# Optimization experiments

Hardware: AMD Instinct MI355X
Metric: run time of the kernel (lower is better)

Reference implementation:

```python
import jax, jax.numpy as jnp
import numpy as np

KSZ = 7
PAD = 3


def setup_inputs() -> dict:
    key = jax.random.key(0)
    ks = jax.random.split(key, 5)
    b, t, c, h, w = 8, 16, 256, 28, 28
    x = jax.random.normal(ks[0], (b, t, c, h, w), dtype=jnp.float32)
    W1 = jax.random.normal(ks[1], (2 * t, t), dtype=jnp.float32) * 0.1
    W2 = jax.random.normal(ks[2], (KSZ, 2 * t), dtype=jnp.float32) * 0.1
    Wl1 = jax.random.normal(ks[3], (c // 4, c, KSZ), dtype=jnp.float32) * 0.05
    Wl2 = jax.random.normal(ks[4], (c, c // 4, 1), dtype=jnp.float32) * 0.1
    return {"x": x, "W1": W1, "W2": W2, "Wl1": Wl1, "Wl2": Wl2}


def _tam_forward(x, W1, W2, Wl1, Wl2):
    b, t, c, h, w = x.shape
    xp = jnp.transpose(x, (0, 2, 1, 3, 4))  # [b,c,t,h,w]
    pooled = jnp.mean(xp, axis=(3, 4))       # [b,c,t] (adaptive_avg_pool2d to 1x1)

    # G branch: per-(b,c) dynamic 7-tap softmax kernel
    g = jnp.tanh(jnp.einsum('bct,ut->bcu', pooled, W1))
    kernel = jax.nn.softmax(jnp.einsum('bcu,ku->bck', g, W2), axis=-1)  # [b,c,7]

    # L branch: conv1d(c -> c/4, k=7, pad=3) -> tanh -> conv1d(c/4 -> c, k=1) -> sigmoid
    y = jax.lax.conv_general_dilated(
        pooled, Wl1, window_strides=(1,), padding=[(PAD, PAD)],
        dimension_numbers=('NCH', 'OIH', 'NCH'))
    y = jnp.tanh(y)  # [b, c/4, t]
    local = jax.nn.sigmoid(jnp.einsum('oi,bit->bot', Wl2[:, :, 0], y))  # [b,c,t]

    gated = xp * local[:, :, :, None, None]  # [b,c,t,h,w]

    # Depthwise temporal conv (groups = b*c), stride 1, pad 3 on t
    padded = jnp.pad(gated, ((0, 0), (0, 0), (PAD, PAD), (0, 0), (0, 0)))
    out = jnp.zeros_like(gated)
    for k in range(KSZ):
        out = out + kernel[:, :, k, None, None, None] * padded[:, :, k:k + t]
    out = jnp.transpose(out, (0, 2, 1, 3, 4))  # [b,t,c,h,w]
    return out.reshape(b * t, c, h, w)


def reference(x, W1, W2, Wl1, Wl2):
    return _tam_forward(x, W1, W2, Wl1, Wl2)
```

## Files before the change

### kernel.cpp

```cpp
#include <hip/hip_runtime.h>

constexpr int B_  = 8;
constexpr int T_  = 16;
constexpr int C_  = 256;
constexpr int HW_ = 784;
constexpr int CO_ = 64;
constexpr int K_  = 7;
constexpr int U2_ = 32;

typedef float floatx4 __attribute__((ext_vector_type(4)));

__device__ __forceinline__ float rfl(float v) {
    return __int_as_float(__builtin_amdgcn_readfirstlane(__float_as_int(v)));
}

__global__ __launch_bounds__(256) void pool_kernel(const float* __restrict__ x,
                                                   float* __restrict__ pooled) {
    int bid  = blockIdx.x;
    int cg   = bid & 63;
    int bt   = bid >> 6;
    int t    = bt & 15;
    int b    = bt >> 4;
    int wave = threadIdx.x >> 6;
    int lane = threadIdx.x & 63;
    int c    = cg * 4 + wave;

    const floatx4* p4 = (const floatx4*)(x + ((size_t)bt * C_ + c) * HW_);
    float s = 0.f;
    for (int j = lane; j < 196; j += 64) {
        floatx4 v = p4[j];
        s += (v.x + v.y) + (v.z + v.w);
    }
#pragma unroll
    for (int m = 32; m >= 1; m >>= 1) s += __shfl_xor(s, m, 64);
    if (lane == 0) pooled[((size_t)b * C_ + c) * T_ + t] = s * (1.0f / 784.0f);
}

__global__ __launch_bounds__(256) void ty_kernel(const float* __restrict__ pooled,
                                                 const float* __restrict__ Wl1,
                                                 float* __restrict__ ty) {
    int b = blockIdx.x / CO_;
    int o = blockIdx.x % CO_;
    __shared__ float pld[T_ * 257];

    int tid = threadIdx.x;
    for (int idx = tid; idx < C_ * T_; idx += 256) {
        int i  = idx >> 4;
        int tt = idx & 15;
        pld[tt * 257 + i] = pooled[((size_t)b * C_ + i) * T_ + tt];
    }
    __syncthreads();

    int t = tid >> 4;
    int q = tid & 15;
    const float* wrow = Wl1 + (size_t)o * (C_ * K_);
    float acc = 0.f;
    for (int j = 0; j < 16; ++j) {
        int i = j * 16 + q;
        const float* wp = wrow + i * K_;
#pragma unroll
        for (int k = 0; k < K_; ++k) {
            int tt = t + k - 3;
            if (tt >= 0 && tt < T_) acc += wp[k] * pld[tt * 257 + i];
        }
    }
    acc += __shfl_xor(acc, 1, 64);
    acc += __shfl_xor(acc, 2, 64);
    acc += __shfl_xor(acc, 4, 64);
    acc += __shfl_xor(acc, 8, 64);
    if (q == 0) ty[((size_t)b * CO_ + o) * T_ + t] = tanhf(acc);
}

__global__ __launch_bounds__(256) void stream_coef_kernel(const float* __restrict__ x,
                                                          const float* __restrict__ pooled,
                                                          const float* __restrict__ ty,
                                                          const float* __restrict__ W1,
                                                          const float* __restrict__ W2,
                                                          const float* __restrict__ Wl2,
                                                          float* __restrict__ out) {
    int bc = blockIdx.x;
    int b  = bc >> 8;
    int c  = bc & 255;
    int tid = threadIdx.x;
    bool active = tid < 196;

    const size_t chan = ((size_t)(b * T_) * C_ + c) * HW_ + (size_t)tid * 4;
    const float* xb = x + chan;
    float*       ob = out + chan;
    const size_t ts = (size_t)C_ * HW_;

    floatx4 w[11];
    if (active) {
#pragma unroll
        for (int tp = 0; tp < 11; ++tp)
            w[tp] = *(const floatx4*)(xb + (size_t)tp * ts);
    }

    __shared__ float loc_s[T_];
    __shared__ float g_s[U2_];
    __shared__ float s_s[8];
    __shared__ float kw_s[8];

    {
        int t = tid >> 4, q = tid & 15;
        float acc = 0.f;
#pragma unroll
        for (int jj = 0; jj < 4; ++jj) {
            int o = q + jj * 16;
            acc += Wl2[(size_t)c * CO_ + o] * ty[((size_t)b * CO_ + o) * T_ + t];
        }
        acc += __shfl_xor(acc, 1, 64);
        acc += __shfl_xor(acc, 2, 64);
        acc += __shfl_xor(acc, 4, 64);
        acc += __shfl_xor(acc, 8, 64);
        if (q == 0) loc_s[t] = 1.0f / (1.0f + __expf(-acc));
    }
    if (tid < U2_) {
        float acc = 0.f;
#pragma unroll
        for (int t2 = 0; t2 < T_; ++t2)
            acc += pooled[(size_t)bc * T_ + t2] * W1[tid * T_ + t2];
        g_s[tid] = tanhf(acc);
    }
    __syncthreads();
    if (tid < K_) {
        float acc = 0.f;
#pragma unroll
        for (int u = 0; u < U2_; ++u) acc += g_s[u] * W2[tid * U2_ + u];
        s_s[tid] = acc;
    }
    __syncthreads();
    if (tid == 0) {
        float m = s_s[0];
#pragma unroll
        for (int k = 1; k < K_; ++k) m = fmaxf(m, s_s[k]);
        float e[K_], sum = 0.f;
#pragma unroll
        for (int k = 0; k < K_; ++k) { e[k] = __expf(s_s[k] - m); sum += e[k]; }
        float inv = 1.0f / sum;
#pragma unroll
        for (int k = 0; k < K_; ++k) kw_s[k] = e[k] * inv;
    }
    __syncthreads();

    float kw[K_], lc[T_];
#pragma unroll
    for (int k = 0; k < K_; ++k) kw[k] = rfl(kw_s[k]);
#pragma unroll
    for (int t = 0; t < T_; ++t) lc[t] = rfl(loc_s[t]);

    if (!active) return;

#pragma unroll
    for (int tp = 0; tp < 11; ++tp) w[tp] *= lc[tp];

#pragma unroll
    for (int t = 0; t < 8; ++t) {
        floatx4 acc = {0.f, 0.f, 0.f, 0.f};
#pragma unroll
        for (int d = -3; d <= 3; ++d) {
            int tp = t + d;
            if (tp >= 0 && tp <= 10) acc += kw[d + 3] * w[tp];
        }
        __builtin_nontemporal_store(acc, (floatx4*)(ob + (size_t)t * ts));
    }

#pragma unroll
    for (int j = 0; j < 6; ++j) w[j] = w[5 + j];
#pragma unroll
    for (int tp = 11; tp < 16; ++tp)
        w[tp - 5] = *(const floatx4*)(xb + (size_t)tp * ts) * lc[tp];

#pragma unroll
    for (int t = 8; t < 16; ++t) {
        floatx4 acc = {0.f, 0.f, 0.f, 0.f};
#pragma unroll
        for (int d = -3; d <= 3; ++d) {
            int tp = t + d;
            if (tp <= 15) acc += kw[d + 3] * w[tp - 5];
        }
        __builtin_nontemporal_store(acc, (floatx4*)(ob + (size_t)t * ts));
    }
}

extern "C" void kernel_launch(void* const* d_in, const int* in_sizes, int n_in,
                              void* d_out, int out_size, void* d_ws, size_t ws_size,
                              hipStream_t stream) {
    const float* x   = (const float*)d_in[0];
    const float* W1  = (const float*)d_in[1];
    const float* W2  = (const float*)d_in[2];
    const float* Wl1 = (const float*)d_in[3];
    const float* Wl2 = (const float*)d_in[4];
    float* out = (float*)d_out;

    float* pooled = (float*)d_ws;
    float* ty     = pooled + B_ * C_ * T_;

    pool_kernel<<<B_ * T_ * (C_ / 4), 256, 0, stream>>>(x, pooled);
    ty_kernel<<<B_ * CO_, 256, 0, stream>>>(pooled, Wl1, ty);
    stream_coef_kernel<<<B_ * C_, 256, 0, stream>>>(x, pooled, ty, W1, W2, Wl2, out);
}
```

Before: 68.66 us.

## Precompute softmax taps in ty kernel and split stream over two time halves

```diff
diff --git a/kernel.cpp b/kernel.cpp
--- a/kernel.cpp
+++ b/kernel.cpp
@@ -36,72 +36,106 @@
     if (lane == 0) pooled[((size_t)b * C_ + c) * T_ + t] = s * (1.0f / 784.0f);
 }
 
-__global__ __launch_bounds__(256) void ty_kernel(const float* __restrict__ pooled,
-                                                 const float* __restrict__ Wl1,
-                                                 float* __restrict__ ty) {
-    int b = blockIdx.x / CO_;
-    int o = blockIdx.x % CO_;
-    __shared__ float pld[T_ * 257];
-
+__global__ __launch_bounds__(256) void ty_kw_kernel(const float* __restrict__ pooled,
+                                                    const float* __restrict__ Wl1,
+                                                    const float* __restrict__ W1,
+                                                    const float* __restrict__ W2,
+                                                    float* __restrict__ ty,
+                                                    float* __restrict__ P) {
     int tid = threadIdx.x;
-    for (int idx = tid; idx < C_ * T_; idx += 256) {
-        int i  = idx >> 4;
-        int tt = idx & 15;
-        pld[tt * 257 + i] = pooled[((size_t)b * C_ + i) * T_ + tt];
-    }
-    __syncthreads();
-
-    int t = tid >> 4;
-    int q = tid & 15;
-    const float* wrow = Wl1 + (size_t)o * (C_ * K_);
-    float acc = 0.f;
-    for (int j = 0; j < 16; ++j) {
-        int i = j * 16 + q;
-        const float* wp = wrow + i * K_;
-#pragma unroll
-        for (int k = 0; k < K_; ++k) {
-            int tt = t + k - 3;
-            if (tt >= 0 && tt < T_) acc += wp[k] * pld[tt * 257 + i];
-        }
-    }
-    acc += __shfl_xor(acc, 1, 64);
-    acc += __shfl_xor(acc, 2, 64);
-    acc += __shfl_xor(acc, 4, 64);
-    acc += __shfl_xor(acc, 8, 64);
-    if (q == 0) ty[((size_t)b * CO_ + o) * T_ + t] = tanhf(acc);
-}
-
-__global__ __launch_bounds__(256) void stream_coef_kernel(const float* __restrict__ x,
-                                                          const float* __restrict__ pooled,
-                                                          const float* __restrict__ ty,
-                                                          const float* __restrict__ W1,
-                                                          const float* __restrict__ W2,
-                                                          const float* __restrict__ Wl2,
-                                                          float* __restrict__ out) {
+    if (blockIdx.x < 512) {
+        int b = blockIdx.x / CO_;
+        int o = blockIdx.x % CO_;
+        __shared__ float pld[T_ * 257];
+
+        for (int idx = tid; idx < C_ * T_; idx += 256) {
+            int i  = idx >> 4;
+            int tt = idx & 15;
+            pld[tt * 257 + i] = pooled[((size_t)b * C_ + i) * T_ + tt];
+        }
+        __syncthreads();
+
+        int t = tid >> 4;
+        int q = tid & 15;
+        const float* wrow = Wl1 + (size_t)o * (C_ * K_);
+        float acc = 0.f;
+        for (int j = 0; j < 16; ++j) {
+            int i = j * 16 + q;
+            const float* wp = wrow + i * K_;
+#pragma unroll
+            for (int k = 0; k < K_; ++k) {
+                int tt = t + k - 3;
+                if (tt >= 0 && tt < T_) acc += wp[k] * pld[tt * 257 + i];
+            }
+        }
+        acc += __shfl_xor(acc, 1, 64);
+        acc += __shfl_xor(acc, 2, 64);
+        acc += __shfl_xor(acc, 4, 64);
+        acc += __shfl_xor(acc, 8, 64);
+        if (q == 0) ty[((size_t)b * CO_ + o) * T_ + t] = tanhf(acc);
+    } else {
+        int bc = blockIdx.x - 512;
+        __shared__ float g_s[U2_];
+        __shared__ float s_s[8];
+        if (tid < U2_) {
+            float acc = 0.f;
+#pragma unroll
+            for (int t2 = 0; t2 < T_; ++t2)
+                acc += pooled[(size_t)bc * T_ + t2] * W1[tid * T_ + t2];
+            g_s[tid] = tanhf(acc);
+        }
+        __syncthreads();
+        if (tid < K_) {
+            float acc = 0.f;
+#pragma unroll
+            for (int u = 0; u < U2_; ++u) acc += g_s[u] * W2[tid * U2_ + u];
+            s_s[tid] = acc;
+        }
+        __syncthreads();
+        if (tid == 0) {
+            float m = s_s[0];
+#pragma unroll
+            for (int k = 1; k < K_; ++k) m = fmaxf(m, s_s[k]);
+            float e[K_], sum = 0.f;
+#pragma unroll
+            for (int k = 0; k < K_; ++k) { e[k] = __expf(s_s[k] - m); sum += e[k]; }
+            float inv = 1.0f / sum;
+            float* prow = P + (size_t)bc * 8;
+#pragma unroll
+            for (int k = 0; k < K_; ++k) prow[k] = e[k] * inv;
+            prow[7] = 0.f;
+        }
+    }
+}
+
+__global__ __launch_bounds__(448) void stream_kernel(const float* __restrict__ x,
+                                                     const float* __restrict__ P,
+                                                     const float* __restrict__ ty,
+                                                     const float* __restrict__ Wl2,
+                                                     float* __restrict__ out) {
     int bc = blockIdx.x;
     int b  = bc >> 8;
     int c  = bc & 255;
     int tid = threadIdx.x;
-    bool active = tid < 196;
-
-    const size_t chan = ((size_t)(b * T_) * C_ + c) * HW_ + (size_t)tid * 4;
+    int half = tid / 196;
+    int col  = tid - half * 196;
+    bool active = half < 2;
+    int w0 = half * 5;
+
+    const size_t ts = (size_t)C_ * HW_;
+    const size_t chan = ((size_t)(b * T_) * C_ + c) * HW_ + (size_t)col * 4;
     const float* xb = x + chan;
     float*       ob = out + chan;
-    const size_t ts = (size_t)C_ * HW_;
 
     floatx4 w[11];
     if (active) {
 #pragma unroll
-        for (int tp = 0; tp < 11; ++tp)
-            w[tp] = *(const floatx4*)(xb + (size_t)tp * ts);
+        for (int j = 0; j < 11; ++j)
+            w[j] = *(const floatx4*)(xb + (size_t)(w0 + j) * ts);
     }
 
     __shared__ float loc_s[T_];
-    __shared__ float g_s[U2_];
-    __shared__ float s_s[8];
-    __shared__ float kw_s[8];
-
-    {
+    if (tid < 256) {
         int t = tid >> 4, q = tid & 15;
         float acc = 0.f;
 #pragma unroll
@@ -115,71 +149,43 @@
         acc += __shfl_xor(acc, 8, 64);
         if (q == 0) loc_s[t] = 1.0f / (1.0f + __expf(-acc));
     }
-    if (tid < U2_) {
-        float acc = 0.f;
-#pragma unroll
-        for (int t2 = 0; t2 < T_; ++t2)
-            acc += pooled[(size_t)bc * T_ + t2] * W1[tid * T_ + t2];
-        g_s[tid] = tanhf(acc);
-    }
     __syncthreads();
-    if (tid < K_) {
-        float acc = 0.f;
-#pragma unroll
-        for (int u = 0; u < U2_; ++u) acc += g_s[u] * W2[tid * U2_ + u];
-        s_s[tid] = acc;
-    }
-    __syncthreads();
-    if (tid == 0) {
-        float m = s_s[0];
-#pragma unroll
-        for (int k = 1; k < K_; ++k) m = fmaxf(m, s_s[k]);
-        float e[K_], sum = 0.f;
-#pragma unroll
-        for (int k = 0; k < K_; ++k) { e[k] = __expf(s_s[k] - m); sum += e[k]; }
-        float inv = 1.0f / sum;
-#pragma unroll
-        for (int k = 0; k < K_; ++k) kw_s[k] = e[k] * inv;
-    }
-    __syncthreads();
-
+
+    const float* prow = P + (size_t)bc * 8;
     float kw[K_], lc[T_];
 #pragma unroll
-    for (int k = 0; k < K_; ++k) kw[k] = rfl(kw_s[k]);
+    for (int k = 0; k < K_; ++k) kw[k] = rfl(prow[k]);
 #pragma unroll
     for (int t = 0; t < T_; ++t) lc[t] = rfl(loc_s[t]);
 
     if (!active) return;
 
 #pragma unroll
-    for (int tp = 0; tp < 11; ++tp) w[tp] *= lc[tp];
-
-#pragma unroll
-    for (int t = 0; t < 8; ++t) {
-        floatx4 acc = {0.f, 0.f, 0.f, 0.f};
-#pragma unroll
-        for (int d = -3; d <= 3; ++d) {
-            int tp = t + d;
-            if (tp >= 0 && tp <= 10) acc += kw[d + 3] * w[tp];
-        }
-        __builtin_nontemporal_store(acc, (floatx4*)(ob + (size_t)t * ts));
-    }
-
-#pragma unroll
-    for (int j = 0; j < 6; ++j) w[j] = w[5 + j];
-#pragma unroll
-    for (int tp = 11; tp < 16; ++tp)
-        w[tp - 5] = *(const floatx4*)(xb + (size_t)tp * ts) * lc[tp];
-
-#pragma unroll
-    for (int t = 8; t < 16; ++t) {
-        floatx4 acc = {0.f, 0.f, 0.f, 0.f};
-#pragma unroll
-        for (int d = -3; d <= 3; ++d) {
-            int tp = t + d;
-            if (tp <= 15) acc += kw[d + 3] * w[tp - 5];
-        }
-        __builtin_nontemporal_store(acc, (floatx4*)(ob + (size_t)t * ts));
+    for (int j = 0; j < 11; ++j) w[j] *= lc[w0 + j];
+
+    if (half == 0) {
+#pragma unroll
+        for (int t = 0; t < 8; ++t) {
+            floatx4 acc = {0.f, 0.f, 0.f, 0.f};
+#pragma unroll
+            for (int d = -3; d <= 3; ++d) {
+                int tp = t + d;
+                if (tp >= 0 && tp <= 10) acc += kw[d + 3] * w[tp];
+            }
+            __builtin_nontemporal_store(acc, (floatx4*)(ob + (size_t)t * ts));
+        }
+    } else {
+#pragma unroll
+        for (int i = 0; i < 8; ++i) {
+            int t = 8 + i;
+            floatx4 acc = {0.f, 0.f, 0.f, 0.f};
+#pragma unroll
+            for (int d = -3; d <= 3; ++d) {
+                int tp = t + d;
+                if (tp <= 15) acc += kw[d + 3] * w[tp - 5];
+            }
+            __builtin_nontemporal_store(acc, (floatx4*)(ob + (size_t)t * ts));
+        }
     }
 }
 
@@ -195,8 +201,9 @@
 
     float* pooled = (float*)d_ws;
     float* ty     = pooled + B_ * C_ * T_;
+    float* P      = ty + B_ * CO_ * T_;
 
     pool_kernel<<<B_ * T_ * (C_ / 4), 256, 0, stream>>>(x, pooled);
-    ty_kernel<<<B_ * CO_, 256, 0, stream>>>(pooled, Wl1, ty);
-    stream_coef_kernel<<<B_ * C_, 256, 0, stream>>>(x, pooled, ty, W1, W2, Wl2, out);
-}
+    ty_kw_kernel<<<512 + B_ * C_, 256, 0, stream>>>(pooled, Wl1, W1, W2, ty, P);
+    stream_kernel<<<B_ * C_, 448, 0, stream>>>(x, P, ty, Wl2, out);
+}
```

Measured after the change: 71.16 us. 1.04x slower.
